# Optimization experiments

Hardware: AMD Instinct MI355X
Metric: run time of the kernel (lower is better)

## Reference

```python
import jax, jax.numpy as jnp
import numpy as np

D = 1024      # neural_dim
M = 8192      # memory_size (assumed fully used)
H = 16        # num_heads
B = 64        # batch
HD = D // H   # head dim


def setup_inputs() -> dict:
    key = jax.random.key(0)
    ks = jax.random.split(key, 24)
    s = 0.02
    inp = {
        "neural_input": jax.random.normal(ks[0], (B, D), jnp.float32),
        "memory_keys": jax.random.normal(ks[1], (M, D), jnp.float32),
        "memory_values": jax.random.normal(ks[2], (M, D), jnp.float32),
        # query/key/value projections (nn.Linear weights are [out, in])
        "Wq": jax.random.normal(ks[3], (D, D), jnp.float32) * s,
        "bq": jnp.zeros((D,), jnp.float32),
        "Wk": jax.random.normal(ks[4], (D, D), jnp.float32) * s,
        "bk": jnp.zeros((D,), jnp.float32),
        "Wv": jax.random.normal(ks[5], (D, D), jnp.float32) * s,
        "bv": jnp.zeros((D,), jnp.float32),
        # MultiheadAttention packed in-projection [3D, D] and out projection
        "in_proj_w": jax.random.normal(ks[6], (3 * D, D), jnp.float32) * s,
        "in_proj_b": jnp.zeros((3 * D,), jnp.float32),
        "out_w": jax.random.normal(ks[7], (D, D), jnp.float32) * s,
        "out_b": jnp.zeros((D,), jnp.float32),
        # memory_gate: Linear(2D->D), ReLU, Linear(D->D), Sigmoid
        "gW1": jax.random.normal(ks[8], (D, 2 * D), jnp.float32) * s,
        "gb1": jnp.zeros((D,), jnp.float32),
        "gW2": jax.random.normal(ks[9], (D, D), jnp.float32) * s,
        "gb2": jnp.zeros((D,), jnp.float32),
        # integration: Linear(2D->2D), ReLU, Linear(2D->D)
        "iW1": jax.random.normal(ks[10], (2 * D, 2 * D), jnp.float32) * s,
        "ib1": jnp.zeros((2 * D,), jnp.float32),
        "iW2": jax.random.normal(ks[11], (D, 2 * D), jnp.float32) * s,
        "ib2": jnp.zeros((D,), jnp.float32),
    }
    return inp


def reference(neural_input, memory_keys, memory_values,
              Wq, bq, Wk, bk, Wv, bv,
              in_proj_w, in_proj_b, out_w, out_b,
              gW1, gb1, gW2, gb2, iW1, ib1, iW2, ib2):
    x = neural_input  # [B, D]
    # pre-projections (memory_used assumed all True -> full tables)
    q = x @ Wq.T + bq                  # [B, D]
    k = memory_keys @ Wk.T + bk        # [M, D]
    v = memory_values @ Wv.T + bv      # [M, D]

    # MultiheadAttention (single query per batch element; K/V shared
    # across batch instead of the redundant expand in the original)
    Wiq, Wik, Wiv = in_proj_w[:D], in_proj_w[D:2 * D], in_proj_w[2 * D:]
    biq, bik, biv = in_proj_b[:D], in_proj_b[D:2 * D], in_proj_b[2 * D:]
    qh = (q @ Wiq.T + biq).reshape(B, H, HD)   # [B, H, hd]
    kh = (k @ Wik.T + bik).reshape(M, H, HD)   # [M, H, hd]
    vh = (v @ Wiv.T + biv).reshape(M, H, HD)   # [M, H, hd]

    scale = 1.0 / np.sqrt(HD).astype(np.float32)
    scores = jnp.einsum('bhd,mhd->bhm', qh, kh) * scale  # [B, H, M]
    attn = jax.nn.softmax(scores, axis=-1)
    ctx = jnp.einsum('bhm,mhd->bhd', attn, vh).reshape(B, D)
    memory_signal = ctx @ out_w.T + out_b      # [B, D]

    # gated fusion
    gate_in = jnp.concatenate([x, memory_signal], axis=-1)          # [B, 2D]
    gate = jax.nn.sigmoid(jax.nn.relu(gate_in @ gW1.T + gb1) @ gW2.T + gb2)
    gated_memory = gate * memory_signal
    combined = jnp.concatenate([x, gated_memory], axis=-1)          # [B, 2D]
    out = jax.nn.relu(combined @ iW1.T + ib1) @ iW2.T + ib2         # [B, D]
    return out
```

## Files before the change

kernel.cpp:

```cpp
#include <hip/hip_runtime.h>
#include <hip/hip_bf16.h>
#include <stdint.h>


typedef __bf16 bf16;
typedef __bf16 bf16x4 __attribute__((ext_vector_type(4)));
typedef __bf16 bf16x8 __attribute__((ext_vector_type(8)));
typedef float f32x4 __attribute__((ext_vector_type(4)));

#define D_ 1024
#define M_ 8192
#define B_ 64
#define H_ 16

static __device__ __forceinline__ void gload16(const void* g, void* l) {
  __builtin_amdgcn_global_load_lds(
      (const __attribute__((address_space(1))) void*)g,
      (__attribute__((address_space(3))) void*)l, 16, 0, 0);
}

static __device__ __forceinline__ f32x4 mfma16(bf16x8 a, bf16x8 b, f32x4 c) {
  return __builtin_amdgcn_mfma_f32_16x16x32_bf16(a, b, c, 0, 0, 0);
}

template <int U, int KLEN, typename OutT>
__device__ __forceinline__ void thin_gemm(
    const bf16* __restrict__ A, int lda,
    const bf16* __restrict__ Bm, int ldb,
    OutT* __restrict__ C, int ldc,
    const float* __restrict__ bias, float scale) {
  const int tid = threadIdx.x, lane = tid & 63, w = tid >> 6;
  const int rl = lane & 15, qq = lane >> 4;
  const bf16* pa = A + (int64_t)(w * 16 + rl) * lda + qq * 8;
  const bf16* pb[4];
  pb[0] = Bm + (int64_t)rl * ldb + qq * 8;
  pb[1] = pb[0] + (int64_t)16 * ldb;
  pb[2] = pb[0] + (int64_t)32 * ldb;
  pb[3] = pb[0] + (int64_t)48 * ldb;
  f32x4 acc[4] = {};
  bf16x8 av[2][U], bv[2][U][4];
#pragma unroll
  for (int u = 0; u < U; u++) {
    av[0][u] = *(const bf16x8*)(pa + u * 32);
#pragma unroll
    for (int j = 0; j < 4; j++)
      bv[0][u][j] = *(const bf16x8*)(pb[j] + u * 32);
  }
  constexpr int NI = KLEN / (32 * U);
#pragma unroll
  for (int it = 0; it < NI; it++) {
    const int cur = it & 1, nxt = cur ^ 1;
    if (it + 1 < NI) {
      int k = (it + 1) * 32 * U;
#pragma unroll
      for (int u = 0; u < U; u++) {
        av[nxt][u] = *(const bf16x8*)(pa + k + u * 32);
#pragma unroll
        for (int j = 0; j < 4; j++)
          bv[nxt][u][j] = *(const bf16x8*)(pb[j] + k + u * 32);
      }
    }
#pragma unroll
    for (int u = 0; u < U; u++)
#pragma unroll
      for (int j = 0; j < 4; j++)
        acc[j] = mfma16(av[cur][u], bv[cur][u][j], acc[j]);
  }
#pragma unroll
  for (int j = 0; j < 4; j++) {
    int gn = j * 16 + rl;
    float bb = bias ? bias[gn] : 0.0f;
#pragma unroll
    for (int r = 0; r < 4; r++) {
      int gm = w * 16 + qq * 4 + r;
      C[(int64_t)gm * ldc + gn] = (OutT)((acc[j][r] + bb) * scale);
    }
  }
}

struct CvtD { const float* src; bf16* dst; int end; };
struct PrepArgs {
  CvtD d[10];
  const float *Wk, *Wv, *inw, *inb, *bq, *bk, *bv;
  const float *outb, *gb1, *gb2, *ib1, *ib2;
  bf16* WT;
  float *bc, *msR, *g1R, *gateR, *h1R, *out, *Oraw, *lmat;
};

__global__ __launch_bounds__(256) void prep_kernel(PrepArgs a) {
  const int bx = blockIdx.x, tid = threadIdx.x;
  if (bx < 7696) {
    int g = bx * 256 + tid;
    CvtD dd = a.d[9];
    int begin = a.d[8].end;
#pragma unroll
    for (int t = 8; t >= 0; t--)
      if (g < a.d[t].end) { dd = a.d[t]; begin = t ? a.d[t - 1].end : 0; }
    int i = (g - begin) * 16;
#pragma unroll
    for (int u = 0; u < 4; u++) {
      float4 v = *(const float4*)(dd.src + i + u * 4);
      bf16x4 o = { (bf16)v.x, (bf16)v.y, (bf16)v.z, (bf16)v.w };
      *(bf16x4*)(dd.dst + i + u * 4) = o;
    }
  } else if (bx < 9744) {
    int t = bx - 7696;
    int z = t >> 10, rem = t & 1023;
    const float* src = z == 0 ? a.Wk : a.Wv;
    bf16* out = a.WT + (int64_t)(z + 1) * D_ * D_;
    __shared__ bf16 tile[32][33];
    int tx = tid & 31, ty = tid >> 5;
    int r0 = (rem >> 5) * 32, c0 = (rem & 31) * 32;
#pragma unroll
    for (int i = 0; i < 32; i += 8)
      tile[ty + i][tx] = (bf16)src[(int64_t)(r0 + ty + i) * D_ + c0 + tx];
    __syncthreads();
#pragma unroll
    for (int i = 0; i < 32; i += 8)
      out[(int64_t)(c0 + ty + i) * D_ + r0 + tx] = tile[tx][ty + i];
  } else if (bx < 10512) {
    int t = bx - 9744;
    int w = tid >> 6, lane = tid & 63;
    int ng = t * 4 + w;
    int z = ng >> 10;
    const float* Wi = a.inw + (int64_t)ng * D_;
    const float* b = z == 0 ? a.bq : z == 1 ? a.bk : a.bv;
    float acc = 0.f;
#pragma unroll
    for (int l = 0; l < D_; l += 64) acc += Wi[l + lane] * b[l + lane];
#pragma unroll
    for (int m = 32; m; m >>= 1) acc += __shfl_xor(acc, m, 64);
    if (lane == 0) a.bc[ng] = acc + a.inb[ng];
  } else if (bx < 10896) {
    int t = bx - 10512;
    int seg = t >> 6, row = t & 63;
    int n = tid * 4;
    const float* b;
    float* dst;
    int bn = n;
    if (seg == 0)      { dst = a.msR   + row * 1024;        b = a.outb; }
    else if (seg == 1) { dst = a.g1R   + row * 1024;        b = a.gb1;  }
    else if (seg == 2) { dst = a.gateR + row * 1024;        b = a.gb2;  }
    else if (seg == 3) { dst = a.h1R   + row * 2048;        b = a.ib1;  }
    else if (seg == 4) { dst = a.h1R   + row * 2048 + 1024; b = a.ib1; bn = 1024 + n; }
    else               { dst = a.out   + row * 1024;        b = a.ib2;  }
    *(float4*)(dst + n) = *(const float4*)(b + bn);
  } else {
    int b = bx - 10896;
    float4 z4 = {0.f, 0.f, 0.f, 0.f};
    *(float4*)(a.Oraw + b * 1024 + tid * 4) = z4;
    if (b < 16 && tid < 64) a.lmat[b * 64 + tid] = 0.f;
  }
}

__global__ __launch_bounds__(256) void gemm_l2(
    const bf16* __restrict__ inpj,
    const bf16* __restrict__ WT,
    float* __restrict__ Wcp,
    const bf16* __restrict__ xbf, const bf16* __restrict__ Wqb,
    bf16* __restrict__ q1) {
  const int bid = blockIdx.x;
  if (bid >= 512) {
    int n0q = (bid - 512) * 64;
    thin_gemm<2, 1024, bf16>(xbf, D_, Wqb + (int64_t)n0q * D_, D_,
                             q1 + n0q, D_, nullptr, 1.0f);
    return;
  }
  const int n0 = (bid & 7) * 128;
  const int m0 = ((bid >> 3) & 7) * 128;
  const int zc = bid >> 6;
  const int z = zc >> 2, kc = zc & 3;
  const bf16* A = inpj + (int64_t)(z + 1) * D_ * D_ + kc * 256;
  const bf16* Bm = WT + (int64_t)(z + 1) * D_ * D_ + kc * 256;
  float* C = Wcp + (int64_t)zc * D_ * D_;

  __shared__ alignas(16) bf16 As[128 * 32];
  __shared__ alignas(16) bf16 Bs[128 * 32];
  const int tid = threadIdx.x, lane = tid & 63, w = tid >> 6;
  const int wm = (w & 1) * 64, wn = (w >> 1) * 64;
  const int rl = lane & 15, qq = lane >> 4;
  f32x4 acc[4][4] = {};

  int c0 = w * 64 + lane, c1 = (4 + w) * 64 + lane;
  int ra0 = c0 >> 2, qa0 = (c0 & 3) ^ ((ra0 >> 1) & 3);
  int ra1 = c1 >> 2, qa1 = (c1 & 3) ^ ((ra1 >> 1) & 3);
  const bf16* gA0 = A + (int64_t)(m0 + ra0) * D_ + qa0 * 8;
  const bf16* gA1 = A + (int64_t)(m0 + ra1) * D_ + qa1 * 8;
  const bf16* gB0 = Bm + (int64_t)(n0 + ra0) * D_ + qa0 * 8;
  const bf16* gB1 = Bm + (int64_t)(n0 + ra1) * D_ + qa1 * 8;
  bf16* lA0 = As + w * 512;
  bf16* lA1 = As + (4 + w) * 512;
  bf16* lB0 = Bs + w * 512;
  bf16* lB1 = Bs + (4 + w) * 512;

  for (int k0 = 0; k0 < 256; k0 += 32) {
    __syncthreads();
    gload16(gA0 + k0, lA0);
    gload16(gA1 + k0, lA1);
    gload16(gB0 + k0, lB0);
    gload16(gB1 + k0, lB1);
    __syncthreads();
    bf16x8 af[4], bb[4];
#pragma unroll
    for (int i = 0; i < 4; i++) {
      int r = wm + i * 16 + rl;
      af[i] = *(const bf16x8*)(As + r * 32 + (qq ^ ((r >> 1) & 3)) * 8);
    }
#pragma unroll
    for (int j = 0; j < 4; j++) {
      int r = wn + j * 16 + rl;
      bb[j] = *(const bf16x8*)(Bs + r * 32 + (qq ^ ((r >> 1) & 3)) * 8);
    }
#pragma unroll
    for (int i = 0; i < 4; i++)
#pragma unroll
      for (int j = 0; j < 4; j++)
        acc[i][j] = mfma16(af[i], bb[j], acc[i][j]);
  }
#pragma unroll
  for (int j = 0; j < 4; j++) {
    int gn = n0 + wn + j * 16 + rl;
#pragma unroll
    for (int i = 0; i < 4; i++) {
      int gm0 = m0 + wm + i * 16 + qq * 4;
#pragma unroll
      for (int r = 0; r < 4; r++)
        C[(int64_t)(gm0 + r) * D_ + gn] = acc[i][j][r];
    }
  }
}

__global__ __launch_bounds__(256) void cvt_wc(
    const float* __restrict__ Wcp, bf16* __restrict__ Wc) {
  const int z = blockIdx.x >> 10, b = blockIdx.x & 1023;
  const int i = (b * 256 + threadIdx.x) * 4;
  const float* p = Wcp + (int64_t)(z * 4) * D_ * D_ + i;
  float4 s = *(const float4*)p;
#pragma unroll
  for (int kc = 1; kc < 4; kc++) {
    float4 t = *(const float4*)(p + (int64_t)kc * D_ * D_);
    s.x += t.x; s.y += t.y; s.z += t.z; s.w += t.w;
  }
  bf16x4 o = { (bf16)s.x, (bf16)s.y, (bf16)s.z, (bf16)s.w };
  *(bf16x4*)(Wc + (int64_t)(z + 1) * D_ * D_ + i) = o;
}

__global__ __launch_bounds__(512) void gemm256(
    const bf16* __restrict__ A,
    const bf16* __restrict__ Wc,
    const float* __restrict__ bc,
    bf16* __restrict__ kh, bf16* __restrict__ vhT,
    const bf16* __restrict__ qA, const bf16* __restrict__ qB,
    bf16* __restrict__ qC, const float* __restrict__ qbias) {
  extern __shared__ __align__(16) bf16 lds[];
  const int bid = blockIdx.x;
  if (bid >= 256) {
    if (threadIdx.x < 256) {
      int n0q = (bid - 256) * 64;
      thin_gemm<2, 1024, bf16>(qA, D_, qB + (int64_t)n0q * D_, D_,
                               qC + n0q, D_, qbias + n0q, 0.125f);
    }
    return;
  }
  const int lin = bid;
  const int xcd = lin & 7, s = lin >> 3;
  const int z = xcd >> 2;
  const int m0 = ((xcd & 3) * 8 + (s >> 2)) * 256;
  const int n0 = (s & 3) * 256;
  const bf16* Ab = A + (int64_t)z * M_ * D_;
  const bf16* Bb = Wc + (int64_t)(z + 1) * D_ * D_;
  const float* bias = bc + (z + 1) * D_;

  const int tid = threadIdx.x, lane = tid & 63, w = tid >> 6;
  const int rl = lane & 15, qq = lane >> 4;
  const int wr = w >> 2, wcn = w & 3;

  const int ci0 = w * 128 + lane, ci1 = ci0 + 64;
  const int ra0 = ci0 >> 2, ca0 = (ci0 & 3) ^ ((ra0 >> 1) & 3);
  const int ra1 = ci1 >> 2, ca1 = (ci1 & 3) ^ ((ra1 >> 1) & 3);
  const bf16* gA0 = Ab + (int64_t)(m0 + ra0) * D_ + ca0 * 8;
  const bf16* gA1 = Ab + (int64_t)(m0 + ra1) * D_ + ca1 * 8;
  const bf16* gB0 = Bb + (int64_t)(n0 + ra0) * D_ + ca0 * 8;
  const bf16* gB1 = Bb + (int64_t)(n0 + ra1) * D_ + ca1 * 8;
  const int lA0 = w * 1024, lA1 = lA0 + 512;

  f32x4 acc[8][4] = {};
  bf16x8 bfr[4], afr[4];
  const int sq8 = (qq ^ ((rl >> 1) & 3)) * 8;

#define SCB __builtin_amdgcn_sched_barrier(0)
#define BARR __builtin_amdgcn_s_barrier()
#define VMW(N) asm volatile("s_waitcnt vmcnt(" #N ")")

#define STAGE_FULL(BUF, KT)                          \
  do {                                               \
    bf16* bse_ = lds + (BUF) * 16384;                \
    gload16(gA0 + (KT) * 32, bse_ + lA0);            \
    gload16(gA1 + (KT) * 32, bse_ + lA1);            \
    gload16(gB0 + (KT) * 32, bse_ + 8192 + lA0);     \
    gload16(gB1 + (KT) * 32, bse_ + 8192 + lA1);     \
  } while (0)

#define PH_A(BUF, DOSTAGE, SKT)                                              \
  do {                                                                       \
    const bf16* ba_ = lds + (BUF) * 16384;                                   \
    const bf16* bb_ = ba_ + 8192;                                            \
    for (int j = 0; j < 4; j++)                                              \
      bfr[j] = *(const bf16x8*)(bb_ + (wcn * 64 + j * 16 + rl) * 32 + sq8);  \
    for (int mi = 0; mi < 4; mi++)                                           \
      afr[mi] = *(const bf16x8*)(ba_ + (wr * 128 + mi * 16 + rl) * 32 + sq8);\
    if (DOSTAGE) {                                                           \
      bf16* bse_ = lds + ((SKT) & 3) * 16384;                                \
      gload16(gA0 + (SKT) * 32, bse_ + lA0);                                 \
      gload16(gA1 + (SKT) * 32, bse_ + lA1);                                 \
    }                                                                        \
    SCB; BARR; SCB;                                                          \
    __builtin_amdgcn_s_setprio(1);                                           \
    for (int mi = 0; mi < 4; mi++)                                           \
      for (int j = 0; j < 4; j++)                                            \
        acc[mi][j] = mfma16(afr[mi], bfr[j], acc[mi][j]);                    \
    __builtin_amdgcn_s_setprio(0);                                           \
    SCB; BARR; SCB;                                                          \
  } while (0)

#define PH_B(BUF, DOSTAGE, SKT, VMSTMT)                                      \
  do {                                                                       \
    const bf16* ba_ = lds + (BUF) * 16384;                                   \
    for (int mi = 0; mi < 4; mi++)                                           \
      afr[mi] =                                                              \
          *(const bf16x8*)(ba_ + (wr * 128 + (mi + 4) * 16 + rl) * 32 + sq8);\
    if (DOSTAGE) {                                                           \
      bf16* bse_ = lds + ((SKT) & 3) * 16384;                                \
      gload16(gB0 + (SKT) * 32, bse_ + 8192 + lA0);                          \
      gload16(gB1 + (SKT) * 32, bse_ + 8192 + lA1);                          \
    }                                                                        \
    VMSTMT;                                                                  \
    SCB; BARR; SCB;                                                          \
    __builtin_amdgcn_s_setprio(1);                                           \
    for (int mi = 0; mi < 4; mi++)                                           \
      for (int j = 0; j < 4; j++)                                            \
        acc[mi + 4][j] = mfma16(afr[mi], bfr[j], acc[mi + 4][j]);            \
    __builtin_amdgcn_s_setprio(0);                                           \
    SCB; BARR; SCB;                                                          \
  } while (0)

  STAGE_FULL(0, 0);
  STAGE_FULL(1, 1);
  STAGE_FULL(2, 2);
  VMW(8);
  SCB; BARR; SCB;

#pragma unroll 1
  for (int t = 0; t < 7; t++) {
    const int kb = t * 4;
    PH_A(0, 1, kb + 3); PH_B(0, 1, kb + 3, VMW(8));
    PH_A(1, 1, kb + 4); PH_B(1, 1, kb + 4, VMW(8));
    PH_A(2, 1, kb + 5); PH_B(2, 1, kb + 5, VMW(8));
    PH_A(3, 1, kb + 6); PH_B(3, 1, kb + 6, VMW(8));
  }
  PH_A(0, 1, 31); PH_B(0, 1, 31, VMW(8));
  PH_A(1, 0, 0);  PH_B(1, 0, 0, VMW(4));
  PH_A(2, 0, 0);  PH_B(2, 0, 0, VMW(0));
  PH_A(3, 0, 0);  PH_B(3, 0, 0, (void)0);

#undef SCB
#undef BARR
#undef VMW
#undef STAGE_FULL
#undef PH_A
#undef PH_B

  if (z == 0) {
#pragma unroll
    for (int j = 0; j < 4; j++) {
      int gn = n0 + wcn * 64 + j * 16 + rl;
      float bb2 = bias[gn];
#pragma unroll
      for (int mi = 0; mi < 8; mi++) {
        int gm0 = m0 + wr * 128 + mi * 16 + qq * 4;
#pragma unroll
        for (int r = 0; r < 4; r++)
          kh[(int64_t)(gm0 + r) * D_ + gn] = (bf16)(acc[mi][j][r] + bb2);
      }
    }
  } else {
#pragma unroll
    for (int j = 0; j < 4; j++) {
      int gn = n0 + wcn * 64 + j * 16 + rl;
      float bb2 = bias[gn];
#pragma unroll
      for (int mi = 0; mi < 8; mi++) {
        int gm0 = m0 + wr * 128 + mi * 16 + qq * 4;
        f32x4 a = acc[mi][j];
        bf16x4 o = { (bf16)(a[0] + bb2), (bf16)(a[1] + bb2),
                     (bf16)(a[2] + bb2), (bf16)(a[3] + bb2) };
        *(bf16x4*)(vhT + (int64_t)gn * M_ + gm0) = o;
      }
    }
  }
}

__global__ __launch_bounds__(256, 2) void flash_kernel(
    const bf16* __restrict__ qh, const bf16* __restrict__ kh,
    const bf16* __restrict__ vhT, float* __restrict__ Oraw,
    float* __restrict__ lmat) {
  const int tid = threadIdx.x, lane = tid & 63, w = tid >> 6;
  const int rl = lane & 15, qq = lane >> 4;
  const int h = blockIdx.x >> 4, c = blockIdx.x & 15;
  __shared__ alignas(16) bf16 Plds[4 * 16 * 72];
  const bf16* qhp = qh + (int64_t)(w * 16 + rl) * D_ + h * 64 + qq * 8;
  bf16x8 aq0 = *(const bf16x8*)(qhp);
  bf16x8 aq1 = *(const bf16x8*)(qhp + 32);
  float lsum[4] = {0.f, 0.f, 0.f, 0.f};
  f32x4 acc_o[4] = {};
  bf16* pl = Plds + w * 1152;
  const bf16* khb = kh + (int64_t)(c * 512) * D_ + h * 64 + qq * 8;
  const bf16* vtb = vhT + (int64_t)(h * 64) * M_ + c * 512 + qq * 8;
  for (int nt = 0; nt < 8; nt++) {
    int mb = nt * 64;
    bf16x8 bk0[4], bk1[4], vv0[4], vv1[4];
#pragma unroll
    for (int j = 0; j < 4; j++) {
      const bf16* p = khb + (int64_t)(mb + j * 16 + rl) * D_;
      bk0[j] = *(const bf16x8*)(p);
      bk1[j] = *(const bf16x8*)(p + 32);
      const bf16* q = vtb + (int64_t)(j * 16 + rl) * M_ + mb;
      vv0[j] = *(const bf16x8*)(q);
      vv1[j] = *(const bf16x8*)(q + 32);
    }
    f32x4 s[4] = {};
#pragma unroll
    for (int j = 0; j < 4; j++) {
      s[j] = mfma16(aq0, bk0[j], s[j]);
      s[j] = mfma16(aq1, bk1[j], s[j]);
    }
#pragma unroll
    for (int j = 0; j < 4; j++)
#pragma unroll
      for (int r = 0; r < 4; r++) {
        float p = __expf(s[j][r]);
        lsum[r] += p;
        pl[(qq * 4 + r) * 72 + j * 16 + rl] = (bf16)p;
      }
    bf16x8 pa0 = *(const bf16x8*)(pl + rl * 72 + qq * 8);
    bf16x8 pa1 = *(const bf16x8*)(pl + rl * 72 + 32 + qq * 8);
#pragma unroll
    for (int j = 0; j < 4; j++) {
      acc_o[j] = mfma16(pa0, vv0[j], acc_o[j]);
      acc_o[j] = mfma16(pa1, vv1[j], acc_o[j]);
    }
  }
#pragma unroll
  for (int msk = 1; msk <= 8; msk <<= 1)
#pragma unroll
    for (int r = 0; r < 4; r++) lsum[r] += __shfl_xor(lsum[r], msk, 64);
#pragma unroll
  for (int j = 0; j < 4; j++)
#pragma unroll
    for (int r = 0; r < 4; r++)
      atomicAdd(&Oraw[(int64_t)(w * 16 + qq * 4 + r) * D_ + h * 64 + j * 16 + rl],
                acc_o[j][r]);
  if (rl == 0)
#pragma unroll
    for (int r = 0; r < 4; r++)
      atomicAdd(&lmat[h * 64 + w * 16 + qq * 4 + r], lsum[r]);
}

struct Chunk { const void* p0; const void* p1; int ld; int kind; };
struct StageArgs { Chunk c[16]; };

template <int NKK>
__global__ __launch_bounds__(256) void tail_stage(
    StageArgs sa, const bf16* __restrict__ Bw, int ldb,
    float* __restrict__ Craw, int ldc) {
  const int n0 = blockIdx.x * 64, kc = blockIdx.y;
  const int bk0 = kc * NKK * 32;
  const Chunk ch = sa.c[kc];
  const int tid = threadIdx.x, lane = tid & 63, w = tid >> 6;
  const int rl = lane & 15, qq = lane >> 4;
  const int m = w * 16 + rl;
  const bf16* pb[4];
#pragma unroll
  for (int j = 0; j < 4; j++)
    pb[j] = Bw + (int64_t)(n0 + j * 16 + rl) * ldb + bk0 + qq * 8;
  f32x4 acc[4] = {};
#pragma unroll
  for (int kk = 0; kk < NKK; kk++) {
    bf16x8 af;
    if (ch.kind == 0) {
      af = *(const bf16x8*)((const bf16*)ch.p0 + (int64_t)m * ch.ld +
                            kk * 32 + qq * 8);
    } else {
      const float* p = (const float*)ch.p0 + (int64_t)m * ch.ld + kk * 32 + qq * 8;
      float4 u0 = *(const float4*)p;
      float4 u1 = *(const float4*)(p + 4);
      if (ch.kind == 2) {
        u0.x = fmaxf(u0.x, 0.f); u0.y = fmaxf(u0.y, 0.f);
        u0.z = fmaxf(u0.z, 0.f); u0.w = fmaxf(u0.w, 0.f);
        u1.x = fmaxf(u1.x, 0.f); u1.y = fmaxf(u1.y, 0.f);
        u1.z = fmaxf(u1.z, 0.f); u1.w = fmaxf(u1.w, 0.f);
      } else if (ch.kind == 3) {
        const float* pm = (const float*)ch.p1 + (int64_t)m * ch.ld + kk * 32 + qq * 8;
        float4 m0 = *(const float4*)pm;
        float4 m1 = *(const float4*)(pm + 4);
        u0.x = m0.x / (1.f + __expf(-u0.x)); u0.y = m0.y / (1.f + __expf(-u0.y));
        u0.z = m0.z / (1.f + __expf(-u0.z)); u0.w = m0.w / (1.f + __expf(-u0.w));
        u1.x = m1.x / (1.f + __expf(-u1.x)); u1.y = m1.y / (1.f + __expf(-u1.y));
        u1.z = m1.z / (1.f + __expf(-u1.z)); u1.w = m1.w / (1.f + __expf(-u1.w));
      } else if (ch.kind == 4) {
        int hidx = (bk0 + kk * 32) >> 6;
        float linv = 1.0f / ((const float*)ch.p1)[hidx * 64 + m];
        u0.x *= linv; u0.y *= linv; u0.z *= linv; u0.w *= linv;
        u1.x *= linv; u1.y *= linv; u1.z *= linv; u1.w *= linv;
      }
      af = (bf16x8){ (bf16)u0.x, (bf16)u0.y, (bf16)u0.z, (bf16)u0.w,
                     (bf16)u1.x, (bf16)u1.y, (bf16)u1.z, (bf16)u1.w };
    }
    bf16x8 bf_[4];
#pragma unroll
    for (int j = 0; j < 4; j++) bf_[j] = *(const bf16x8*)(pb[j] + kk * 32);
#pragma unroll
    for (int j = 0; j < 4; j++) acc[j] = mfma16(af, bf_[j], acc[j]);
  }
#pragma unroll
  for (int j = 0; j < 4; j++) {
    int gn = n0 + j * 16 + rl;
#pragma unroll
    for (int r = 0; r < 4; r++) {
      int gm = w * 16 + qq * 4 + r;
      atomicAdd(&Craw[(int64_t)gm * ldc + gn], acc[j][r]);
    }
  }
}

extern "C" void kernel_launch(void* const* d_in, const int* in_sizes, int n_in,
                              void* d_out, int out_size, void* d_ws,
                              size_t ws_size, hipStream_t stream) {
  (void)in_sizes; (void)n_in; (void)out_size;
  const float* x    = (const float*)d_in[0];
  const float* mk   = (const float*)d_in[1];
  const float* mv   = (const float*)d_in[2];
  const float* Wq   = (const float*)d_in[3];
  const float* bq   = (const float*)d_in[4];
  const float* Wk   = (const float*)d_in[5];
  const float* bk   = (const float*)d_in[6];
  const float* Wv   = (const float*)d_in[7];
  const float* bv   = (const float*)d_in[8];
  const float* inw  = (const float*)d_in[9];
  const float* inb  = (const float*)d_in[10];
  const float* outw = (const float*)d_in[11];
  const float* outb = (const float*)d_in[12];
  const float* gW1  = (const float*)d_in[13];
  const float* gb1  = (const float*)d_in[14];
  const float* gW2  = (const float*)d_in[15];
  const float* gb2  = (const float*)d_in[16];
  const float* iW1  = (const float*)d_in[17];
  const float* ib1  = (const float*)d_in[18];
  const float* iW2  = (const float*)d_in[19];
  const float* ib2  = (const float*)d_in[20];

  char* ws = (char*)d_ws;
  size_t off = 0;
  auto alloc = [&](size_t bytes) {
    char* p = ws + off;
    off += (bytes + 255) & ~(size_t)255;
    return p;
  };
  bf16* mkmv  = (bf16*)alloc((size_t)2 * M_ * D_ * 2);
  bf16* inpj  = (bf16*)alloc((size_t)3 * D_ * D_ * 2);
  bf16* WT    = (bf16*)alloc((size_t)3 * D_ * D_ * 2);
  bf16* Wc    = (bf16*)alloc((size_t)3 * D_ * D_ * 2);
  float* bc   = (float*)alloc(3 * D_ * 4);
  bf16* xbf   = (bf16*)alloc((size_t)B_ * D_ * 2);
  bf16* qh    = (bf16*)alloc((size_t)B_ * D_ * 2);
  bf16* kh    = (bf16*)alloc((size_t)M_ * D_ * 2);
  bf16* vhT   = (bf16*)alloc((size_t)M_ * D_ * 2);
  float* Oraw = (float*)alloc((size_t)B_ * D_ * 4);
  float* lmat = (float*)alloc((size_t)H_ * B_ * 4);
  float* msR  = (float*)alloc((size_t)B_ * D_ * 4);
  float* g1R  = (float*)alloc((size_t)B_ * D_ * 4);
  float* gateR= (float*)alloc((size_t)B_ * D_ * 4);
  float* h1R  = (float*)alloc((size_t)B_ * 2 * D_ * 4);
  bf16* gW1b  = (bf16*)alloc((size_t)D_ * 2 * D_ * 2);
  bf16* gW2b  = (bf16*)alloc((size_t)D_ * D_ * 2);
  bf16* iW1b  = (bf16*)alloc((size_t)2 * D_ * 2 * D_ * 2);
  bf16* iW2b  = (bf16*)alloc((size_t)D_ * 2 * D_ * 2);
  bf16* outwb = (bf16*)alloc((size_t)D_ * D_ * 2);
  bf16* Wqb   = (bf16*)alloc((size_t)D_ * D_ * 2);
  bf16* q1    = (bf16*)alloc((size_t)B_ * D_ * 2);
  if (ws_size < off) return;
  float* Wcp = (float*)kh;

  PrepArgs pa;
  pa.d[0] = { mk,   mkmv,           524288 };
  pa.d[1] = { mv,   mkmv + M_ * D_, 1048576 };
  pa.d[2] = { inw,  inpj,           1245184 };
  pa.d[3] = { gW1,  gW1b,           1376256 };
  pa.d[4] = { gW2,  gW2b,           1441792 };
  pa.d[5] = { iW1,  iW1b,           1703936 };
  pa.d[6] = { iW2,  iW2b,           1835008 };
  pa.d[7] = { outw, outwb,          1900544 };
  pa.d[8] = { Wq,   Wqb,            1966080 };
  pa.d[9] = { x,    xbf,            1970176 };
  pa.Wk = Wk; pa.Wv = Wv; pa.inw = inw; pa.inb = inb;
  pa.bq = bq; pa.bk = bk; pa.bv = bv;
  pa.outb = outb; pa.gb1 = gb1; pa.gb2 = gb2; pa.ib1 = ib1; pa.ib2 = ib2;
  pa.WT = WT; pa.bc = bc; pa.msR = msR; pa.g1R = g1R; pa.gateR = gateR;
  pa.h1R = h1R; pa.out = (float*)d_out; pa.Oraw = Oraw; pa.lmat = lmat;
  prep_kernel<<<dim3(10960), 256, 0, stream>>>(pa);

  gemm_l2<<<dim3(528), 256, 0, stream>>>(inpj, WT, Wcp, xbf, Wqb, q1);

  cvt_wc<<<dim3(2048), 256, 0, stream>>>(Wcp, Wc);

  hipFuncSetAttribute((const void*)gemm256,
                      hipFuncAttributeMaxDynamicSharedMemorySize, 131072);
  gemm256<<<dim3(272), dim3(512), 131072, stream>>>(
      mkmv, Wc, bc, kh, vhT, q1, inpj, qh, bc);

  flash_kernel<<<dim3(256), 256, 0, stream>>>(qh, kh, vhT, Oraw, lmat);

  StageArgs s1;
  for (int kc = 0; kc < 8; kc++) s1.c[kc] = { Oraw + kc * 128, lmat, D_, 4 };
  tail_stage<4><<<dim3(16, 8), 256, 0, stream>>>(s1, outwb, D_, msR, D_);

  StageArgs s2;
  for (int kc = 0; kc < 8; kc++)  s2.c[kc] = { xbf + kc * 128, nullptr, D_, 0 };
  for (int kc = 8; kc < 16; kc++) s2.c[kc] = { msR + (kc - 8) * 128, nullptr, D_, 1 };
  tail_stage<4><<<dim3(16, 16), 256, 0, stream>>>(s2, gW1b, 2 * D_, g1R, D_);

  StageArgs s3;
  for (int kc = 0; kc < 8; kc++) s3.c[kc] = { g1R + kc * 128, nullptr, D_, 2 };
  tail_stage<4><<<dim3(16, 8), 256, 0, stream>>>(s3, gW2b, D_, gateR, D_);

  StageArgs s4;
  for (int kc = 0; kc < 8; kc++)  s4.c[kc] = { xbf + kc * 128, nullptr, D_, 0 };
  for (int kc = 8; kc < 16; kc++)
    s4.c[kc] = { gateR + (kc - 8) * 128, msR + (kc - 8) * 128, D_, 3 };
  tail_stage<4><<<dim3(32, 16), 256, 0, stream>>>(s4, iW1b, 2 * D_, h1R, 2 * D_);

  StageArgs s5;
  for (int kc = 0; kc < 16; kc++) s5.c[kc] = { h1R + kc * 128, nullptr, 2 * D_, 2 };
  tail_stage<4><<<dim3(16, 16), 256, 0, stream>>>(s5, iW2b, 2 * D_,
                                                  (float*)d_out, D_);
}
```

Baseline: 360.0 us.

## Fold Wq into combined weight GEMM and overlap bulk conversions with it

The query projection Wq is now transposed and folded into a third combined weight product (Wiq·Wq), so q is computed in a single thin GEMM from x instead of two chained ones. The split-K fp32 weight-combine GEMM plus its separate reduction kernel is replaced by a full-K GEMM that writes bf16 directly, which removes the fp32 partial buffers and one launch. The large memory-table and tail-weight fp32→bf16 conversions move out of the prep kernel into extra blocks of the GEMM launch, so they can run alongside the GEMM, using wider 32-element-per-thread conversion blocks. In exchange, the GEMM has fewer, longer blocks (192 full-K tiles instead of 512 split-K), and rounding changes slightly because Wq is pre-multiplied.

```diff
diff --git a/kernel.cpp b/kernel.cpp
--- a/kernel.cpp
+++ b/kernel.cpp
@@ -21,6 +21,28 @@
 
 static __device__ __forceinline__ f32x4 mfma16(bf16x8 a, bf16x8 b, f32x4 c) {
   return __builtin_amdgcn_mfma_f32_16x16x32_bf16(a, b, c, 0, 0, 0);
+}
+
+struct CvtD { const float* src; bf16* dst; int end; };
+
+template <int N>
+static __device__ __forceinline__ void cvt_block(const CvtD* d, int b, int tid) {
+  CvtD dd = d[N - 1];
+  int begin = N > 1 ? d[N - 2].end : 0;
+#pragma unroll
+  for (int t = N - 2; t >= 0; t--)
+    if (b < d[t].end) { dd = d[t]; begin = t ? d[t - 1].end : 0; }
+  int64_t i = (int64_t)(b - begin) * 8192 + tid * 32;
+  const float* src = dd.src + i;
+  bf16* dst = dd.dst + i;
+  float4 v[8];
+#pragma unroll
+  for (int u = 0; u < 8; u++) v[u] = *(const float4*)(src + u * 4);
+#pragma unroll
+  for (int u = 0; u < 8; u++) {
+    bf16x4 o = { (bf16)v[u].x, (bf16)v[u].y, (bf16)v[u].z, (bf16)v[u].w };
+    *(bf16x4*)(dst + u * 4) = o;
+  }
 }
 
 template <int U, int KLEN, typename OutT>
@@ -78,10 +100,9 @@
   }
 }
 
-struct CvtD { const float* src; bf16* dst; int end; };
 struct PrepArgs {
-  CvtD d[10];
-  const float *Wk, *Wv, *inw, *inb, *bq, *bk, *bv;
+  CvtD d[2];
+  const float *Wq, *Wk, *Wv, *inw, *inb, *bq, *bk, *bv;
   const float *outb, *gb1, *gb2, *ib1, *ib2;
   bf16* WT;
   float *bc, *msR, *g1R, *gateR, *h1R, *out, *Oraw, *lmat;
@@ -89,25 +110,13 @@
 
 __global__ __launch_bounds__(256) void prep_kernel(PrepArgs a) {
   const int bx = blockIdx.x, tid = threadIdx.x;
-  if (bx < 7696) {
-    int g = bx * 256 + tid;
-    CvtD dd = a.d[9];
-    int begin = a.d[8].end;
-#pragma unroll
-    for (int t = 8; t >= 0; t--)
-      if (g < a.d[t].end) { dd = a.d[t]; begin = t ? a.d[t - 1].end : 0; }
-    int i = (g - begin) * 16;
-#pragma unroll
-    for (int u = 0; u < 4; u++) {
-      float4 v = *(const float4*)(dd.src + i + u * 4);
-      bf16x4 o = { (bf16)v.x, (bf16)v.y, (bf16)v.z, (bf16)v.w };
-      *(bf16x4*)(dd.dst + i + u * 4) = o;
-    }
-  } else if (bx < 9744) {
-    int t = bx - 7696;
+  if (bx < 392) {
+    cvt_block<2>(a.d, bx, tid);
+  } else if (bx < 3464) {
+    int t = bx - 392;
     int z = t >> 10, rem = t & 1023;
-    const float* src = z == 0 ? a.Wk : a.Wv;
-    bf16* out = a.WT + (int64_t)(z + 1) * D_ * D_;
+    const float* src = z == 0 ? a.Wq : z == 1 ? a.Wk : a.Wv;
+    bf16* out = a.WT + (int64_t)z * D_ * D_;
     __shared__ bf16 tile[32][33];
     int tx = tid & 31, ty = tid >> 5;
     int r0 = (rem >> 5) * 32, c0 = (rem & 31) * 32;
@@ -118,8 +127,8 @@
 #pragma unroll
     for (int i = 0; i < 32; i += 8)
       out[(int64_t)(c0 + ty + i) * D_ + r0 + tx] = tile[tx][ty + i];
-  } else if (bx < 10512) {
-    int t = bx - 9744;
+  } else if (bx < 4232) {
+    int t = bx - 3464;
     int w = tid >> 6, lane = tid & 63;
     int ng = t * 4 + w;
     int z = ng >> 10;
@@ -131,8 +140,8 @@
 #pragma unroll
     for (int m = 32; m; m >>= 1) acc += __shfl_xor(acc, m, 64);
     if (lane == 0) a.bc[ng] = acc + a.inb[ng];
-  } else if (bx < 10896) {
-    int t = bx - 10512;
+  } else if (bx < 4616) {
+    int t = bx - 4232;
     int seg = t >> 6, row = t & 63;
     int n = tid * 4;
     const float* b;
@@ -146,37 +155,29 @@
     else               { dst = a.out   + row * 1024;        b = a.ib2;  }
     *(float4*)(dst + n) = *(const float4*)(b + bn);
   } else {
-    int b = bx - 10896;
+    int b = bx - 4616;
     float4 z4 = {0.f, 0.f, 0.f, 0.f};
     *(float4*)(a.Oraw + b * 1024 + tid * 4) = z4;
     if (b < 16 && tid < 64) a.lmat[b * 64 + tid] = 0.f;
   }
 }
 
-__global__ __launch_bounds__(256) void gemm_l2(
-    const bf16* __restrict__ inpj,
-    const bf16* __restrict__ WT,
-    float* __restrict__ Wcp,
-    const bf16* __restrict__ xbf, const bf16* __restrict__ Wqb,
-    bf16* __restrict__ q1) {
-  const int bid = blockIdx.x;
-  if (bid >= 512) {
-    int n0q = (bid - 512) * 64;
-    thin_gemm<2, 1024, bf16>(xbf, D_, Wqb + (int64_t)n0q * D_, D_,
-                             q1 + n0q, D_, nullptr, 1.0f);
+struct L2Args { CvtD d[7]; };
+
+__global__ __launch_bounds__(256) void gemm_bigc(
+    const bf16* __restrict__ A, const bf16* __restrict__ Bm,
+    bf16* __restrict__ C, L2Args ca) {
+  const int bid = blockIdx.x, tid = threadIdx.x;
+  if (bid >= 192) {
+    cvt_block<7>(ca.d, bid - 192, tid);
     return;
   }
-  const int n0 = (bid & 7) * 128;
-  const int m0 = ((bid >> 3) & 7) * 128;
-  const int zc = bid >> 6;
-  const int z = zc >> 2, kc = zc & 3;
-  const bf16* A = inpj + (int64_t)(z + 1) * D_ * D_ + kc * 256;
-  const bf16* Bm = WT + (int64_t)(z + 1) * D_ * D_ + kc * 256;
-  float* C = Wcp + (int64_t)zc * D_ * D_;
-
+  const int z = bid >> 6, r = bid & 63;
+  const int m0 = (r >> 3) * 128, n0 = (r & 7) * 128;
+  A += (int64_t)z * D_ * D_; Bm += (int64_t)z * D_ * D_;
   __shared__ alignas(16) bf16 As[128 * 32];
   __shared__ alignas(16) bf16 Bs[128 * 32];
-  const int tid = threadIdx.x, lane = tid & 63, w = tid >> 6;
+  const int lane = tid & 63, w = tid >> 6;
   const int wm = (w & 1) * 64, wn = (w >> 1) * 64;
   const int rl = lane & 15, qq = lane >> 4;
   f32x4 acc[4][4] = {};
@@ -193,7 +194,7 @@
   bf16* lB0 = Bs + w * 512;
   bf16* lB1 = Bs + (4 + w) * 512;
 
-  for (int k0 = 0; k0 < 256; k0 += 32) {
+  for (int k0 = 0; k0 < D_; k0 += 32) {
     __syncthreads();
     gload16(gA0 + k0, lA0);
     gload16(gA1 + k0, lA1);
@@ -203,13 +204,13 @@
     bf16x8 af[4], bb[4];
 #pragma unroll
     for (int i = 0; i < 4; i++) {
-      int r = wm + i * 16 + rl;
-      af[i] = *(const bf16x8*)(As + r * 32 + (qq ^ ((r >> 1) & 3)) * 8);
+      int rr = wm + i * 16 + rl;
+      af[i] = *(const bf16x8*)(As + rr * 32 + (qq ^ ((rr >> 1) & 3)) * 8);
     }
 #pragma unroll
     for (int j = 0; j < 4; j++) {
-      int r = wn + j * 16 + rl;
-      bb[j] = *(const bf16x8*)(Bs + r * 32 + (qq ^ ((r >> 1) & 3)) * 8);
+      int rr = wn + j * 16 + rl;
+      bb[j] = *(const bf16x8*)(Bs + rr * 32 + (qq ^ ((rr >> 1) & 3)) * 8);
     }
 #pragma unroll
     for (int i = 0; i < 4; i++)
@@ -217,6 +218,7 @@
       for (int j = 0; j < 4; j++)
         acc[i][j] = mfma16(af[i], bb[j], acc[i][j]);
   }
+  C += (int64_t)z * D_ * D_;
 #pragma unroll
   for (int j = 0; j < 4; j++) {
     int gn = n0 + wn + j * 16 + rl;
@@ -224,25 +226,10 @@
     for (int i = 0; i < 4; i++) {
       int gm0 = m0 + wm + i * 16 + qq * 4;
 #pragma unroll
-      for (int r = 0; r < 4; r++)
-        C[(int64_t)(gm0 + r) * D_ + gn] = acc[i][j][r];
-    }
-  }
-}
-
-__global__ __launch_bounds__(256) void cvt_wc(
-    const float* __restrict__ Wcp, bf16* __restrict__ Wc) {
-  const int z = blockIdx.x >> 10, b = blockIdx.x & 1023;
-  const int i = (b * 256 + threadIdx.x) * 4;
-  const float* p = Wcp + (int64_t)(z * 4) * D_ * D_ + i;
-  float4 s = *(const float4*)p;
-#pragma unroll
-  for (int kc = 1; kc < 4; kc++) {
-    float4 t = *(const float4*)(p + (int64_t)kc * D_ * D_);
-    s.x += t.x; s.y += t.y; s.z += t.z; s.w += t.w;
-  }
-  bf16x4 o = { (bf16)s.x, (bf16)s.y, (bf16)s.z, (bf16)s.w };
-  *(bf16x4*)(Wc + (int64_t)(z + 1) * D_ * D_ + i) = o;
+      for (int r2 = 0; r2 < 4; r2++)
+        C[(int64_t)(gm0 + r2) * D_ + gn] = (bf16)acc[i][j][r2];
+    }
+  }
 }
 
 __global__ __launch_bounds__(512) void gemm256(
@@ -586,37 +573,32 @@
   bf16* iW1b  = (bf16*)alloc((size_t)2 * D_ * 2 * D_ * 2);
   bf16* iW2b  = (bf16*)alloc((size_t)D_ * 2 * D_ * 2);
   bf16* outwb = (bf16*)alloc((size_t)D_ * D_ * 2);
-  bf16* Wqb   = (bf16*)alloc((size_t)D_ * D_ * 2);
-  bf16* q1    = (bf16*)alloc((size_t)B_ * D_ * 2);
   if (ws_size < off) return;
-  float* Wcp = (float*)kh;
 
   PrepArgs pa;
-  pa.d[0] = { mk,   mkmv,           524288 };
-  pa.d[1] = { mv,   mkmv + M_ * D_, 1048576 };
-  pa.d[2] = { inw,  inpj,           1245184 };
-  pa.d[3] = { gW1,  gW1b,           1376256 };
-  pa.d[4] = { gW2,  gW2b,           1441792 };
-  pa.d[5] = { iW1,  iW1b,           1703936 };
-  pa.d[6] = { iW2,  iW2b,           1835008 };
-  pa.d[7] = { outw, outwb,          1900544 };
-  pa.d[8] = { Wq,   Wqb,            1966080 };
-  pa.d[9] = { x,    xbf,            1970176 };
-  pa.Wk = Wk; pa.Wv = Wv; pa.inw = inw; pa.inb = inb;
+  pa.d[0] = { inw, inpj, 384 };
+  pa.d[1] = { x,   xbf,  392 };
+  pa.Wq = Wq; pa.Wk = Wk; pa.Wv = Wv; pa.inw = inw; pa.inb = inb;
   pa.bq = bq; pa.bk = bk; pa.bv = bv;
   pa.outb = outb; pa.gb1 = gb1; pa.gb2 = gb2; pa.ib1 = ib1; pa.ib2 = ib2;
   pa.WT = WT; pa.bc = bc; pa.msR = msR; pa.g1R = g1R; pa.gateR = gateR;
   pa.h1R = h1R; pa.out = (float*)d_out; pa.Oraw = Oraw; pa.lmat = lmat;
-  prep_kernel<<<dim3(10960), 256, 0, stream>>>(pa);
-
-  gemm_l2<<<dim3(528), 256, 0, stream>>>(inpj, WT, Wcp, xbf, Wqb, q1);
-
-  cvt_wc<<<dim3(2048), 256, 0, stream>>>(Wcp, Wc);
+  prep_kernel<<<dim3(4680), 256, 0, stream>>>(pa);
+
+  L2Args ca;
+  ca.d[0] = { mk,   mkmv,           1024 };
+  ca.d[1] = { mv,   mkmv + M_ * D_, 2048 };
+  ca.d[2] = { gW1,  gW1b,           2304 };
+  ca.d[3] = { gW2,  gW2b,           2432 };
+  ca.d[4] = { iW1,  iW1b,           2944 };
+  ca.d[5] = { iW2,  iW2b,           3200 };
+  ca.d[6] = { outw, outwb,          3328 };
+  gemm_bigc<<<dim3(3520), 256, 0, stream>>>(inpj, WT, Wc, ca);
 
   hipFuncSetAttribute((const void*)gemm256,
                       hipFuncAttributeMaxDynamicSharedMemorySize, 131072);
   gemm256<<<dim3(272), dim3(512), 131072, stream>>>(
-      mkmv, Wc, bc, kh, vhT, q1, inpj, qh, bc);
+      mkmv, Wc, bc, kh, vhT, xbf, Wc, qh, bc);
 
   flash_kernel<<<dim3(256), 256, 0, stream>>>(qh, kh, vhT, Oraw, lmat);
 
```

Measured after the change: 330.8 us. 8.1% less time.
